# Optimization experiments

Measured on AMD Instinct MI355X. Metric: run time of the kernel, lower is better.

The kernel has to match this reference:

```python
import jax, jax.numpy as jnp
import numpy as np

EMBED_DIM = 1024
NUM_HEADS = 16
HEAD_DIM = EMBED_DIM // NUM_HEADS


def setup_inputs() -> dict:
    key = jax.random.key(0)
    ks = jax.random.split(key, 9)
    B, S, D = 4, 2048, EMBED_DIM
    scale = 1.0 / np.sqrt(D)
    x = jax.random.normal(ks[0], (B, S, D), dtype=jnp.float32)
    Wq = jax.random.normal(ks[1], (D, D), dtype=jnp.float32) * scale
    bq = jax.random.normal(ks[2], (D,), dtype=jnp.float32) * 0.01
    Wk = jax.random.normal(ks[3], (D, D), dtype=jnp.float32) * scale
    bk = jax.random.normal(ks[4], (D,), dtype=jnp.float32) * 0.01
    Wv = jax.random.normal(ks[5], (D, D), dtype=jnp.float32) * scale
    bv = jax.random.normal(ks[6], (D,), dtype=jnp.float32) * 0.01
    Wo = jax.random.normal(ks[7], (D, D), dtype=jnp.float32) * scale
    bo = jax.random.normal(ks[8], (D,), dtype=jnp.float32) * 0.01
    return {"x": x, "Wq": Wq, "bq": bq, "Wk": Wk, "bk": bk,
            "Wv": Wv, "bv": bv, "Wo": Wo, "bo": bo}


def reference(x, Wq, bq, Wk, bk, Wv, bv, Wo, bo):
    # Self-attention (kv = input). torch Linear: y = x @ W.T + b
    B, S, D = x.shape
    H, Dh = NUM_HEADS, HEAD_DIM
    q = (x @ Wq.T + bq).reshape(B, S, H, Dh).transpose(0, 2, 1, 3)  # [B,H,S,Dh]
    k = (x @ Wk.T + bk).reshape(B, S, H, Dh).transpose(0, 2, 1, 3)
    v = (x @ Wv.T + bv).reshape(B, S, H, Dh).transpose(0, 2, 1, 3)
    scale = 1.0 / jnp.sqrt(jnp.asarray(Dh, dtype=x.dtype))
    scores = jnp.einsum("bhsd,bhtd->bhst", q, k) * scale  # [B,H,S,S]
    causal = jnp.tril(jnp.ones((S, S), dtype=bool))        # True = keep
    scores = jnp.where(causal, scores, jnp.asarray(-jnp.inf, dtype=scores.dtype))
    attn = jax.nn.softmax(scores, axis=-1)
    out = jnp.einsum("bhst,bhtd->bhsd", attn, v)           # [B,H,S,Dh]
    out = out.transpose(0, 2, 1, 3).reshape(B, S, D)
    return out @ Wo.T + bo
```

## Files before the change

kernel.cpp:

```cpp
#include <hip/hip_runtime.h>

#define DMODEL 1024
#define NH     16
#define DH     64
#define BATCH  4
#define SEQ    2048
#define NROWS  (BATCH*SEQ)
#define QTILES (SEQ/256)

typedef short    s16x8  __attribute__((ext_vector_type(8)));
typedef float    f32x4  __attribute__((ext_vector_type(4)));
typedef float    f32x16 __attribute__((ext_vector_type(16)));
typedef unsigned u32x4  __attribute__((ext_vector_type(4)));

#define MFMA16 __builtin_amdgcn_mfma_f32_16x16x32_bf16
#define MFMA32 __builtin_amdgcn_mfma_f32_32x32x16_bf16

__device__ __forceinline__ unsigned short f2bf(float f) {
    unsigned u = __builtin_bit_cast(unsigned, f);
    return (unsigned short)((u + 0x7FFFu + ((u >> 16) & 1u)) >> 16);
}
__device__ __forceinline__ float bf2f(unsigned short s) {
    return __builtin_bit_cast(float, (unsigned)s << 16);
}
__device__ __forceinline__ unsigned pk2(unsigned short a, unsigned short b) {
    return (unsigned)a | ((unsigned)b << 16);
}
__device__ __forceinline__ void split4(float4 v, unsigned& h0, unsigned& h1,
                                       unsigned& l0, unsigned& l1) {
    unsigned short hx=f2bf(v.x), hy=f2bf(v.y), hz=f2bf(v.z), hw=f2bf(v.w);
    h0 = pk2(hx,hy); h1 = pk2(hz,hw);
    l0 = pk2(f2bf(v.x-bf2f(hx)), f2bf(v.y-bf2f(hy)));
    l1 = pk2(f2bf(v.z-bf2f(hz)), f2bf(v.w-bf2f(hw)));
}

#define LDK 40

__global__ __launch_bounds__(256, 2)
void qkv_kernel(const float* __restrict__ x,
                const float* __restrict__ Wq, const float* __restrict__ bq,
                const float* __restrict__ Wk, const float* __restrict__ bk,
                const float* __restrict__ Wv, const float* __restrict__ bv,
                float* __restrict__ qo, float* __restrict__ ko, float* __restrict__ vo)
{
    const int bmi = blockIdx.x;
    const int bn  = blockIdx.y;
    const int mat = bn >> 3;
    const float* __restrict__ W    = (mat == 0) ? Wq : (mat == 1) ? Wk : Wv;
    const float* __restrict__ bias = (mat == 0) ? bq : (mat == 1) ? bk : bv;
    float* __restrict__ out        = (mat == 0) ? qo : (mat == 1) ? ko : vo;
    const int m0 = bmi * 128;
    const int c0 = (bn & 7) * 128;

    __shared__ unsigned short Ah[128][LDK], Al[128][LDK];
    __shared__ unsigned short Bh[128][LDK], Bl[128][LDK];

    const int t    = threadIdx.x;
    const int srow = t >> 1;
    const int skc  = (t & 1) * 16;
    const int lane = t & 63;
    const int wid  = t >> 6;
    const int wm   = (wid >> 1) * 64;
    const int wn   = (wid & 1) * 64;
    const int fr   = lane & 15;
    const int fk   = (lane >> 4) * 8;

    const float* pa = &x[(size_t)(m0 + srow)*DMODEL + skc];
    const float* pb = &W[(size_t)(c0 + srow)*DMODEL + skc];

    f32x4 acc[4][4];
    #pragma unroll
    for (int i = 0; i < 4; ++i)
        #pragma unroll
        for (int j = 0; j < 4; ++j)
            #pragma unroll
            for (int e = 0; e < 4; ++e) acc[i][j][e] = 0.f;

    float4 av[4], bv4[4];
    #pragma unroll
    for (int i = 0; i < 4; ++i) { av[i] = *(const float4*)(pa + 4*i); bv4[i] = *(const float4*)(pb + 4*i); }

    for (int k0 = 0; k0 < DMODEL; k0 += 32) {
        __syncthreads();
        #pragma unroll
        for (int i = 0; i < 4; ++i) {
            unsigned h0,h1,l0,l1;
            split4(av[i], h0,h1,l0,l1);
            *(unsigned*)&Ah[srow][skc+4*i]   = h0;  *(unsigned*)&Ah[srow][skc+4*i+2] = h1;
            *(unsigned*)&Al[srow][skc+4*i]   = l0;  *(unsigned*)&Al[srow][skc+4*i+2] = l1;
            split4(bv4[i], h0,h1,l0,l1);
            *(unsigned*)&Bh[srow][skc+4*i]   = h0;  *(unsigned*)&Bh[srow][skc+4*i+2] = h1;
            *(unsigned*)&Bl[srow][skc+4*i]   = l0;  *(unsigned*)&Bl[srow][skc+4*i+2] = l1;
        }
        __syncthreads();

        const int kn = (k0 + 32 < DMODEL) ? k0 + 32 : 0;
        #pragma unroll
        for (int i = 0; i < 4; ++i) { av[i] = *(const float4*)(pa + kn + 4*i); bv4[i] = *(const float4*)(pb + kn + 4*i); }

        s16x8 a_hi[4], a_lo[4], b_hi[4], b_lo[4];
        #pragma unroll
        for (int i = 0; i < 4; ++i) {
            a_hi[i] = *(const s16x8*)&Ah[wm + i*16 + fr][fk];
            a_lo[i] = *(const s16x8*)&Al[wm + i*16 + fr][fk];
            b_hi[i] = *(const s16x8*)&Bh[wn + i*16 + fr][fk];
            b_lo[i] = *(const s16x8*)&Bl[wn + i*16 + fr][fk];
        }
        #pragma unroll
        for (int i = 0; i < 4; ++i)
            #pragma unroll
            for (int j = 0; j < 4; ++j) {
                acc[i][j] = MFMA16(a_hi[i], b_hi[j], acc[i][j], 0, 0, 0);
                acc[i][j] = MFMA16(a_hi[i], b_lo[j], acc[i][j], 0, 0, 0);
                acc[i][j] = MFMA16(a_lo[i], b_hi[j], acc[i][j], 0, 0, 0);
            }
    }

    const int rbase = m0 + wm + (lane >> 4) * 4;
    #pragma unroll
    for (int j = 0; j < 4; ++j) {
        const int cidx = c0 + wn + j*16 + fr;
        const float bb = bias[cidx];
        const int hd = cidx >> 6;
        const int dh = cidx & 63;
        #pragma unroll
        for (int i = 0; i < 4; ++i)
            #pragma unroll
            for (int r4 = 0; r4 < 4; ++r4) {
                const int r = rbase + i*16 + r4;
                const int b = r >> 11;
                const int s = r & (SEQ - 1);
                out[((size_t)(b*NH + hd)*SEQ + s)*DH + dh] = acc[i][j][r4] + bb;
            }
    }
}

#define LDKK 72
#define LDVT 74

__global__ __launch_bounds__(256, 2)
void attn_kernel(const float* __restrict__ qg, const float* __restrict__ kg,
                 const float* __restrict__ vg, float* __restrict__ out)
{
    const int bx = blockIdx.x, bh = blockIdx.y;
    const int qt = (bh & 32) ? bx : (QTILES - 1 - bx);
    const int t  = threadIdx.x;
    const int w  = t >> 6;
    const int lane = t & 63;
    const int h  = lane >> 5;
    const int c  = lane & 31;
    const int q0 = qt * 256;
    const int wq0 = q0 + w * 64;

    __shared__ unsigned short Kh[64][LDKK], Kl[64][LDKK];
    __shared__ unsigned short Vth[64][LDVT], Vtl[64][LDVT];
    __shared__ float l_lds[4][64];

    s16x8 qfh[2][4], qfl[2][4];
    #pragma unroll
    for (int qrt = 0; qrt < 2; ++qrt)
        #pragma unroll
        for (int s = 0; s < 4; ++s) {
            const float* qp = qg + ((size_t)bh*SEQ + (wq0 + qrt*32 + c))*DH + s*16 + h*8;
            u32x4 hw, lw;
            #pragma unroll
            for (int p2 = 0; p2 < 4; ++p2) {
                const float f0 = 0.125f * qp[2*p2];
                const float f1 = 0.125f * qp[2*p2+1];
                const unsigned short b0 = f2bf(f0), b1 = f2bf(f1);
                hw[p2] = pk2(b0, b1);
                lw[p2] = pk2(f2bf(f0 - bf2f(b0)), f2bf(f1 - bf2f(b1)));
            }
            qfh[qrt][s] = __builtin_bit_cast(s16x8, hw);
            qfl[qrt][s] = __builtin_bit_cast(s16x8, lw);
        }

    f32x16 oacc[2][2];
    #pragma unroll
    for (int i = 0; i < 2; ++i)
        #pragma unroll
        for (int j = 0; j < 2; ++j)
            #pragma unroll
            for (int e = 0; e < 16; ++e) oacc[i][j][e] = 0.f;
    float lsum0 = 0.f, lsum1 = 0.f;

    const float* kbase = kg + (size_t)bh*SEQ*DH;
    const float* vbase = vg + (size_t)bh*SEQ*DH;
    const int wlim = wq0 + 64;

    for (int kb = 0; kb < q0 + 256; kb += 64) {
        __syncthreads();
        const float4* kt4 = (const float4*)(kbase + (size_t)kb*DH);
        #pragma unroll
        for (int i = 0; i < 4; ++i) {
            const int f = t + i*256;
            const int key = f >> 4;
            const int d4  = (f & 15) * 4;
            unsigned h0,h1,l0,l1;
            split4(kt4[f], h0,h1,l0,l1);
            *(unsigned*)&Kh[key][d4]   = h0;  *(unsigned*)&Kh[key][d4+2] = h1;
            *(unsigned*)&Kl[key][d4]   = l0;  *(unsigned*)&Kl[key][d4+2] = l1;
        }
        const float* vt0 = vbase + (size_t)kb*DH;
        #pragma unroll
        for (int j = 0; j < 16; ++j) {
            const int key = w + 4*j;
            const float vv = vt0[(size_t)key*DH + lane];
            const unsigned short hb = f2bf(vv);
            Vth[lane][key] = hb;
            Vtl[lane][key] = f2bf(vv - bf2f(hb));
        }
        __syncthreads();

        if (kb < wlim) {
            f32x16 sac[2][2];
            #pragma unroll
            for (int i = 0; i < 2; ++i)
                #pragma unroll
                for (int j = 0; j < 2; ++j)
                    #pragma unroll
                    for (int e = 0; e < 16; ++e) sac[i][j][e] = 0.f;

            #pragma unroll
            for (int s = 0; s < 4; ++s) {
                s16x8 akh[2], akl[2];
                #pragma unroll
                for (int kt = 0; kt < 2; ++kt) {
                    akh[kt] = *(const s16x8*)&Kh[kt*32 + c][s*16 + h*8];
                    akl[kt] = *(const s16x8*)&Kl[kt*32 + c][s*16 + h*8];
                }
                #pragma unroll
                for (int kt = 0; kt < 2; ++kt)
                    #pragma unroll
                    for (int qrt = 0; qrt < 2; ++qrt) {
                        sac[kt][qrt] = MFMA32(akh[kt], qfh[qrt][s], sac[kt][qrt], 0,0,0);
                        sac[kt][qrt] = MFMA32(akh[kt], qfl[qrt][s], sac[kt][qrt], 0,0,0);
                        sac[kt][qrt] = MFMA32(akl[kt], qfh[qrt][s], sac[kt][qrt], 0,0,0);
                    }
            }

            const bool diag = (kb == wq0);
            float ps0 = 0.f, ps1 = 0.f;
            #pragma unroll
            for (int kt = 0; kt < 2; ++kt)
                #pragma unroll
                for (int qrt = 0; qrt < 2; ++qrt)
                    #pragma unroll
                    for (int r = 0; r < 16; ++r) {
                        float p = __expf(sac[kt][qrt][r] - 8.0f);
                        if (diag) {
                            const int key = kb + kt*32 + (r & 3) + ((r >> 2) << 3) + h*4;
                            const int qr  = wq0 + qrt*32 + c;
                            p = (key <= qr) ? p : 0.f;
                        }
                        sac[kt][qrt][r] = p;
                        if (qrt == 0) ps0 += p; else ps1 += p;
                    }
            lsum0 += ps0; lsum1 += ps1;

            #pragma unroll
            for (int s = 0; s < 4; ++s) {
                const int kt = s >> 1;
                const int rb = (s & 1) * 8;
                s16x8 pfh[2], pfl[2];
                #pragma unroll
                for (int qrt = 0; qrt < 2; ++qrt) {
                    unsigned short ph[8], pl[8];
                    #pragma unroll
                    for (int j = 0; j < 8; ++j) {
                        const float p = sac[kt][qrt][rb + j];
                        const unsigned short hb = f2bf(p);
                        ph[j] = hb;
                        pl[j] = f2bf(p - bf2f(hb));
                    }
                    const unsigned G0h0 = pk2(ph[0],ph[1]), G0h1 = pk2(ph[2],ph[3]);
                    const unsigned G1h0 = pk2(ph[4],ph[5]), G1h1 = pk2(ph[6],ph[7]);
                    const unsigned G0l0 = pk2(pl[0],pl[1]), G0l1 = pk2(pl[2],pl[3]);
                    const unsigned G1l0 = pk2(pl[4],pl[5]), G1l1 = pk2(pl[6],pl[7]);
                    const unsigned sG0h0 = __shfl_xor(G0h0, 32, 64), sG0h1 = __shfl_xor(G0h1, 32, 64);
                    const unsigned sG1h0 = __shfl_xor(G1h0, 32, 64), sG1h1 = __shfl_xor(G1h1, 32, 64);
                    const unsigned sG0l0 = __shfl_xor(G0l0, 32, 64), sG0l1 = __shfl_xor(G0l1, 32, 64);
                    const unsigned sG1l0 = __shfl_xor(G1l0, 32, 64), sG1l1 = __shfl_xor(G1l1, 32, 64);
                    u32x4 fh, fl;
                    if (h == 0) {
                        fh[0]=G0h0;  fh[1]=G0h1;  fh[2]=sG0h0; fh[3]=sG0h1;
                        fl[0]=G0l0;  fl[1]=G0l1;  fl[2]=sG0l0; fl[3]=sG0l1;
                    } else {
                        fh[0]=sG1h0; fh[1]=sG1h1; fh[2]=G1h0;  fh[3]=G1h1;
                        fl[0]=sG1l0; fl[1]=sG1l1; fl[2]=G1l0;  fl[3]=G1l1;
                    }
                    pfh[qrt] = __builtin_bit_cast(s16x8, fh);
                    pfl[qrt] = __builtin_bit_cast(s16x8, fl);
                }
                #pragma unroll
                for (int dt = 0; dt < 2; ++dt) {
                    const unsigned short* vhp = &Vth[dt*32 + c][s*16 + h*8];
                    const unsigned short* vlp = &Vtl[dt*32 + c][s*16 + h*8];
                    u32x4 wh, wl;
                    #pragma unroll
                    for (int u = 0; u < 4; ++u) {
                        wh[u] = *(const unsigned*)(vhp + 2*u);
                        wl[u] = *(const unsigned*)(vlp + 2*u);
                    }
                    const s16x8 vfh = __builtin_bit_cast(s16x8, wh);
                    const s16x8 vfl = __builtin_bit_cast(s16x8, wl);
                    #pragma unroll
                    for (int qrt = 0; qrt < 2; ++qrt) {
                        oacc[qrt][dt] = MFMA32(pfh[qrt], vfh, oacc[qrt][dt], 0,0,0);
                        oacc[qrt][dt] = MFMA32(pfh[qrt], vfl, oacc[qrt][dt], 0,0,0);
                        oacc[qrt][dt] = MFMA32(pfl[qrt], vfh, oacc[qrt][dt], 0,0,0);
                    }
                }
            }
        }
    }

    lsum0 += __shfl_xor(lsum0, 32, 64);
    lsum1 += __shfl_xor(lsum1, 32, 64);
    l_lds[w][c]      = lsum0;
    l_lds[w][32 + c] = lsum1;
    __syncthreads();

    const int b = bh >> 4, hd = bh & 15;
    #pragma unroll
    for (int qrt = 0; qrt < 2; ++qrt)
        #pragma unroll
        for (int r = 0; r < 16; ++r) {
            const int qloc = qrt*32 + (r & 3) + ((r >> 2) << 3) + h*4;
            const float linv = 1.f / l_lds[w][qloc];
            float* op = out + ((size_t)(b*SEQ + wq0 + qloc))*DMODEL + hd*DH;
            op[c]      = oacc[qrt][0][r] * linv;
            op[32 + c] = oacc[qrt][1][r] * linv;
        }
}

__global__ __launch_bounds__(256, 2)
void proj_kernel(const float* __restrict__ A, const float* __restrict__ W,
                 const float* __restrict__ bias, float* __restrict__ out)
{
    const int m0 = blockIdx.x * 128;
    const int c0 = blockIdx.y * 128;

    __shared__ unsigned short Ah[128][LDK], Al[128][LDK];
    __shared__ unsigned short Bh[128][LDK], Bl[128][LDK];

    const int t    = threadIdx.x;
    const int srow = t >> 1;
    const int skc  = (t & 1) * 16;
    const int lane = t & 63;
    const int wid  = t >> 6;
    const int wm   = (wid >> 1) * 64;
    const int wn   = (wid & 1) * 64;
    const int fr   = lane & 15;
    const int fk   = (lane >> 4) * 8;

    const float* pa = &A[(size_t)(m0 + srow)*DMODEL + skc];
    const float* pb = &W[(size_t)(c0 + srow)*DMODEL + skc];

    f32x4 acc[4][4];
    #pragma unroll
    for (int i = 0; i < 4; ++i)
        #pragma unroll
        for (int j = 0; j < 4; ++j)
            #pragma unroll
            for (int e = 0; e < 4; ++e) acc[i][j][e] = 0.f;

    float4 av[4], bv4[4];
    #pragma unroll
    for (int i = 0; i < 4; ++i) { av[i] = *(const float4*)(pa + 4*i); bv4[i] = *(const float4*)(pb + 4*i); }

    for (int k0 = 0; k0 < DMODEL; k0 += 32) {
        __syncthreads();
        #pragma unroll
        for (int i = 0; i < 4; ++i) {
            unsigned h0,h1,l0,l1;
            split4(av[i], h0,h1,l0,l1);
            *(unsigned*)&Ah[srow][skc+4*i]   = h0;  *(unsigned*)&Ah[srow][skc+4*i+2] = h1;
            *(unsigned*)&Al[srow][skc+4*i]   = l0;  *(unsigned*)&Al[srow][skc+4*i+2] = l1;
            split4(bv4[i], h0,h1,l0,l1);
            *(unsigned*)&Bh[srow][skc+4*i]   = h0;  *(unsigned*)&Bh[srow][skc+4*i+2] = h1;
            *(unsigned*)&Bl[srow][skc+4*i]   = l0;  *(unsigned*)&Bl[srow][skc+4*i+2] = l1;
        }
        __syncthreads();

        const int kn = (k0 + 32 < DMODEL) ? k0 + 32 : 0;
        #pragma unroll
        for (int i = 0; i < 4; ++i) { av[i] = *(const float4*)(pa + kn + 4*i); bv4[i] = *(const float4*)(pb + kn + 4*i); }

        s16x8 a_hi[4], a_lo[4], b_hi[4], b_lo[4];
        #pragma unroll
        for (int i = 0; i < 4; ++i) {
            a_hi[i] = *(const s16x8*)&Ah[wm + i*16 + fr][fk];
            a_lo[i] = *(const s16x8*)&Al[wm + i*16 + fr][fk];
            b_hi[i] = *(const s16x8*)&Bh[wn + i*16 + fr][fk];
            b_lo[i] = *(const s16x8*)&Bl[wn + i*16 + fr][fk];
        }
        #pragma unroll
        for (int i = 0; i < 4; ++i)
            #pragma unroll
            for (int j = 0; j < 4; ++j) {
                acc[i][j] = MFMA16(a_hi[i], b_hi[j], acc[i][j], 0, 0, 0);
                acc[i][j] = MFMA16(a_hi[i], b_lo[j], acc[i][j], 0, 0, 0);
                acc[i][j] = MFMA16(a_lo[i], b_hi[j], acc[i][j], 0, 0, 0);
            }
    }

    const int rbase = m0 + wm + (lane >> 4) * 4;
    #pragma unroll
    for (int j = 0; j < 4; ++j) {
        const int cidx = c0 + wn + j*16 + fr;
        const float bb = bias[cidx];
        #pragma unroll
        for (int i = 0; i < 4; ++i)
            #pragma unroll
            for (int r4 = 0; r4 < 4; ++r4) {
                const int r = rbase + i*16 + r4;
                out[(size_t)r*DMODEL + cidx] = acc[i][j][r4] + bb;
            }
    }
}

extern "C" void kernel_launch(void* const* d_in, const int* in_sizes, int n_in,
                              void* d_out, int out_size, void* d_ws, size_t ws_size,
                              hipStream_t stream)
{
    const float* x  = (const float*)d_in[0];
    const float* Wq = (const float*)d_in[1];
    const float* bq = (const float*)d_in[2];
    const float* Wk = (const float*)d_in[3];
    const float* bk = (const float*)d_in[4];
    const float* Wv = (const float*)d_in[5];
    const float* bv = (const float*)d_in[6];
    const float* Wo = (const float*)d_in[7];
    const float* bo = (const float*)d_in[8];
    float* out = (float*)d_out;

    float* ws = (float*)d_ws;
    const size_t SZ = (size_t)NROWS * DMODEL;
    float* q  = ws;
    float* k  = ws + SZ;
    float* v  = ws + 2*SZ;
    float* ao = ws + 3*SZ;

    dim3 g1(NROWS/128, 24);
    qkv_kernel<<<g1, 256, 0, stream>>>(x, Wq, bq, Wk, bk, Wv, bv, q, k, v);

    dim3 g2(QTILES, BATCH*NH);
    attn_kernel<<<g2, 256, 0, stream>>>(q, k, v, ao);

    dim3 g3(NROWS/128, DMODEL/128);
    proj_kernel<<<g3, 256, 0, stream>>>(ao, Wo, bo, out);
}
```

Baseline: 553.0 us.

## Store intermediates as pre-split bf16 hi/lo pairs and double-buffer attention K/V tiles

Adds a pre-pass that splits x into bf16 hi/lo halves. The QKV projection now emits Q, K and a transposed V directly as bf16 hi/lo pairs, and attention writes its output the same way. This removes the repeated fp32-to-bf16 split work inside the GEMM and attention inner loops and lets those loops copy tiles with vector loads. Attention also double-buffers its K/V shared-memory tiles with register prefetch, so it syncs once per iteration, and the 1/8 Q scale moves into the exp argument. The cost is an extra kernel launch, a pass over x, and scattered 2-byte stores for the transposed V.

```diff
diff --git a/kernel.cpp b/kernel.cpp
--- a/kernel.cpp
+++ b/kernel.cpp
@@ -8,65 +8,99 @@
 #define NROWS  (BATCH*SEQ)
 #define QTILES (SEQ/256)
 
+typedef unsigned short u16;
+typedef unsigned int   u32;
 typedef short    s16x8  __attribute__((ext_vector_type(8)));
 typedef float    f32x4  __attribute__((ext_vector_type(4)));
 typedef float    f32x16 __attribute__((ext_vector_type(16)));
 typedef unsigned u32x4  __attribute__((ext_vector_type(4)));
+typedef unsigned u32x2  __attribute__((ext_vector_type(2)));
 
 #define MFMA16 __builtin_amdgcn_mfma_f32_16x16x32_bf16
 #define MFMA32 __builtin_amdgcn_mfma_f32_32x32x16_bf16
 
-__device__ __forceinline__ unsigned short f2bf(float f) {
-    unsigned u = __builtin_bit_cast(unsigned, f);
-    return (unsigned short)((u + 0x7FFFu + ((u >> 16) & 1u)) >> 16);
-}
-__device__ __forceinline__ float bf2f(unsigned short s) {
-    return __builtin_bit_cast(float, (unsigned)s << 16);
-}
-__device__ __forceinline__ unsigned pk2(unsigned short a, unsigned short b) {
-    return (unsigned)a | ((unsigned)b << 16);
-}
-__device__ __forceinline__ void split4(float4 v, unsigned& h0, unsigned& h1,
-                                       unsigned& l0, unsigned& l1) {
-    unsigned short hx=f2bf(v.x), hy=f2bf(v.y), hz=f2bf(v.z), hw=f2bf(v.w);
-    h0 = pk2(hx,hy); h1 = pk2(hz,hw);
-    l0 = pk2(f2bf(v.x-bf2f(hx)), f2bf(v.y-bf2f(hy)));
-    l1 = pk2(f2bf(v.z-bf2f(hz)), f2bf(v.w-bf2f(hw)));
+__device__ __forceinline__ u16 f2bf(float f) {
+    u32 u = __builtin_bit_cast(u32, f);
+    return (u16)((u + 0x7FFFu + ((u >> 16) & 1u)) >> 16);
+}
+__device__ __forceinline__ float bf2f(u16 s) {
+    return __builtin_bit_cast(float, (u32)s << 16);
+}
+__device__ __forceinline__ u32 pk2(u16 a, u16 b) {
+    return (u32)a | ((u32)b << 16);
+}
+__device__ __forceinline__ void split16(const float4* f4, u32x4& h0, u32x4& h1,
+                                        u32x4& l0, u32x4& l1) {
+    float f[16];
+    #pragma unroll
+    for (int i = 0; i < 4; ++i) { f[4*i]=f4[i].x; f[4*i+1]=f4[i].y; f[4*i+2]=f4[i].z; f[4*i+3]=f4[i].w; }
+    u32 hw[8], lw[8];
+    #pragma unroll
+    for (int u = 0; u < 8; ++u) {
+        const u16 a = f2bf(f[2*u]), b = f2bf(f[2*u+1]);
+        hw[u] = pk2(a, b);
+        lw[u] = pk2(f2bf(f[2*u] - bf2f(a)), f2bf(f[2*u+1] - bf2f(b)));
+    }
+    h0 = (u32x4){hw[0],hw[1],hw[2],hw[3]}; h1 = (u32x4){hw[4],hw[5],hw[6],hw[7]};
+    l0 = (u32x4){lw[0],lw[1],lw[2],lw[3]}; l1 = (u32x4){lw[4],lw[5],lw[6],lw[7]};
+}
+
+__global__ __launch_bounds__(256)
+void split_x_kernel(const float* __restrict__ x, u16* __restrict__ xh, u16* __restrict__ xl)
+{
+    const int n4 = NROWS*DMODEL/4;
+    for (int i = blockIdx.x*256 + threadIdx.x; i < n4; i += gridDim.x*256) {
+        const float4 v = ((const float4*)x)[i];
+        float f[4] = {v.x, v.y, v.z, v.w};
+        u32 h[2], l[2];
+        #pragma unroll
+        for (int u = 0; u < 2; ++u) {
+            const u16 a = f2bf(f[2*u]), b = f2bf(f[2*u+1]);
+            h[u] = pk2(a, b);
+            l[u] = pk2(f2bf(f[2*u] - bf2f(a)), f2bf(f[2*u+1] - bf2f(b)));
+        }
+        *(u32x2*)&xh[4*i] = (u32x2){h[0], h[1]};
+        *(u32x2*)&xl[4*i] = (u32x2){l[0], l[1]};
+    }
 }
 
 #define LDK 40
 
 __global__ __launch_bounds__(256, 2)
-void qkv_kernel(const float* __restrict__ x,
+void qkv_kernel(const u16* __restrict__ xh, const u16* __restrict__ xl,
                 const float* __restrict__ Wq, const float* __restrict__ bq,
                 const float* __restrict__ Wk, const float* __restrict__ bk,
                 const float* __restrict__ Wv, const float* __restrict__ bv,
-                float* __restrict__ qo, float* __restrict__ ko, float* __restrict__ vo)
+                u16* __restrict__ qh, u16* __restrict__ ql,
+                u16* __restrict__ kh, u16* __restrict__ kl,
+                u16* __restrict__ vth, u16* __restrict__ vtl)
 {
     const int bmi = blockIdx.x;
     const int bn  = blockIdx.y;
     const int mat = bn >> 3;
     const float* __restrict__ W    = (mat == 0) ? Wq : (mat == 1) ? Wk : Wv;
     const float* __restrict__ bias = (mat == 0) ? bq : (mat == 1) ? bk : bv;
-    float* __restrict__ out        = (mat == 0) ? qo : (mat == 1) ? ko : vo;
     const int m0 = bmi * 128;
     const int c0 = (bn & 7) * 128;
 
-    __shared__ unsigned short Ah[128][LDK], Al[128][LDK];
-    __shared__ unsigned short Bh[128][LDK], Bl[128][LDK];
+    __shared__ u16 Ah[128][LDK], Al[128][LDK];
+    __shared__ u16 Bh[128][LDK], Bl[128][LDK];
 
     const int t    = threadIdx.x;
-    const int srow = t >> 1;
-    const int skc  = (t & 1) * 16;
     const int lane = t & 63;
     const int wid  = t >> 6;
     const int wm   = (wid >> 1) * 64;
     const int wn   = (wid & 1) * 64;
     const int fr   = lane & 15;
     const int fk   = (lane >> 4) * 8;
-
-    const float* pa = &x[(size_t)(m0 + srow)*DMODEL + skc];
-    const float* pb = &W[(size_t)(c0 + srow)*DMODEL + skc];
+    const int ar  = t >> 2;
+    const int ac  = (t & 3) * 8;
+    const int srow = t >> 1;
+    const int skc  = (t & 1) * 16;
+
+    const u16*   pah = &xh[(size_t)(m0 + ar)*DMODEL + ac];
+    const u16*   pal = &xl[(size_t)(m0 + ar)*DMODEL + ac];
+    const float* pb  = &W[(size_t)(c0 + srow)*DMODEL + skc];
 
     f32x4 acc[4][4];
     #pragma unroll
@@ -76,27 +110,36 @@
             #pragma unroll
             for (int e = 0; e < 4; ++e) acc[i][j][e] = 0.f;
 
-    float4 av[4], bv4[4];
-    #pragma unroll
-    for (int i = 0; i < 4; ++i) { av[i] = *(const float4*)(pa + 4*i); bv4[i] = *(const float4*)(pb + 4*i); }
+    u32x4 ra0, ra1, ra2, ra3;
+    float4 rb[4];
+    ra0 = *(const u32x4*)(pah);
+    ra1 = *(const u32x4*)(pah + (size_t)64*DMODEL);
+    ra2 = *(const u32x4*)(pal);
+    ra3 = *(const u32x4*)(pal + (size_t)64*DMODEL);
+    #pragma unroll
+    for (int i = 0; i < 4; ++i) rb[i] = *(const float4*)(pb + 4*i);
 
     for (int k0 = 0; k0 < DMODEL; k0 += 32) {
         __syncthreads();
-        #pragma unroll
-        for (int i = 0; i < 4; ++i) {
-            unsigned h0,h1,l0,l1;
-            split4(av[i], h0,h1,l0,l1);
-            *(unsigned*)&Ah[srow][skc+4*i]   = h0;  *(unsigned*)&Ah[srow][skc+4*i+2] = h1;
-            *(unsigned*)&Al[srow][skc+4*i]   = l0;  *(unsigned*)&Al[srow][skc+4*i+2] = l1;
-            split4(bv4[i], h0,h1,l0,l1);
-            *(unsigned*)&Bh[srow][skc+4*i]   = h0;  *(unsigned*)&Bh[srow][skc+4*i+2] = h1;
-            *(unsigned*)&Bl[srow][skc+4*i]   = l0;  *(unsigned*)&Bl[srow][skc+4*i+2] = l1;
-        }
+        *(u32x4*)&Ah[ar][ac]      = ra0;
+        *(u32x4*)&Ah[ar + 64][ac] = ra1;
+        *(u32x4*)&Al[ar][ac]      = ra2;
+        *(u32x4*)&Al[ar + 64][ac] = ra3;
+        u32x4 h0, h1, l0, l1;
+        split16(rb, h0, h1, l0, l1);
+        *(u32x4*)&Bh[srow][skc]     = h0;
+        *(u32x4*)&Bh[srow][skc + 8] = h1;
+        *(u32x4*)&Bl[srow][skc]     = l0;
+        *(u32x4*)&Bl[srow][skc + 8] = l1;
         __syncthreads();
 
         const int kn = (k0 + 32 < DMODEL) ? k0 + 32 : 0;
-        #pragma unroll
-        for (int i = 0; i < 4; ++i) { av[i] = *(const float4*)(pa + kn + 4*i); bv4[i] = *(const float4*)(pb + kn + 4*i); }
+        ra0 = *(const u32x4*)(pah + kn);
+        ra1 = *(const u32x4*)(pah + kn + (size_t)64*DMODEL);
+        ra2 = *(const u32x4*)(pal + kn);
+        ra3 = *(const u32x4*)(pal + kn + (size_t)64*DMODEL);
+        #pragma unroll
+        for (int i = 0; i < 4; ++i) rb[i] = *(const float4*)(pb + kn + 4*i);
 
         s16x8 a_hi[4], a_lo[4], b_hi[4], b_lo[4];
         #pragma unroll
@@ -130,17 +173,30 @@
                 const int r = rbase + i*16 + r4;
                 const int b = r >> 11;
                 const int s = r & (SEQ - 1);
-                out[((size_t)(b*NH + hd)*SEQ + s)*DH + dh] = acc[i][j][r4] + bb;
-            }
-    }
-}
-
-#define LDKK 72
-#define LDVT 74
+                const float v = acc[i][j][r4] + bb;
+                const u16 hb = f2bf(v);
+                const u16 lb = f2bf(v - bf2f(hb));
+                if (mat == 2) {
+                    const size_t idx = ((size_t)(b*NH + hd)*DH + dh)*SEQ + s;
+                    vth[idx] = hb; vtl[idx] = lb;
+                } else if (mat == 1) {
+                    const size_t idx = ((size_t)(b*NH + hd)*SEQ + s)*DH + dh;
+                    kh[idx] = hb; kl[idx] = lb;
+                } else {
+                    const size_t idx = ((size_t)(b*NH + hd)*SEQ + s)*DH + dh;
+                    qh[idx] = hb; ql[idx] = lb;
+                }
+            }
+    }
+}
+
+#define LDA 72
 
 __global__ __launch_bounds__(256, 2)
-void attn_kernel(const float* __restrict__ qg, const float* __restrict__ kg,
-                 const float* __restrict__ vg, float* __restrict__ out)
+void attn_kernel(const u16* __restrict__ qh, const u16* __restrict__ ql,
+                 const u16* __restrict__ kh, const u16* __restrict__ kl,
+                 const u16* __restrict__ vth, const u16* __restrict__ vtl,
+                 u16* __restrict__ aoh, u16* __restrict__ aol)
 {
     const int bx = blockIdx.x, bh = blockIdx.y;
     const int qt = (bh & 32) ? bx : (QTILES - 1 - bx);
@@ -151,28 +207,25 @@
     const int c  = lane & 31;
     const int q0 = qt * 256;
     const int wq0 = q0 + w * 64;
-
-    __shared__ unsigned short Kh[64][LDKK], Kl[64][LDKK];
-    __shared__ unsigned short Vth[64][LDVT], Vtl[64][LDVT];
+    const int wlim = wq0 + 64;
+
+    __shared__ u16 Kh[2][64][LDA], Kl[2][64][LDA];
+    __shared__ u16 Vh[2][64][LDA], Vl[2][64][LDA];
     __shared__ float l_lds[4][64];
 
+    const int sr = t >> 3;
+    const int sc = (t & 7) * 8;
+    const size_t krow = (size_t)bh * SEQ;
+    const size_t vrow = (size_t)bh * DH;
+
     s16x8 qfh[2][4], qfl[2][4];
     #pragma unroll
     for (int qrt = 0; qrt < 2; ++qrt)
         #pragma unroll
         for (int s = 0; s < 4; ++s) {
-            const float* qp = qg + ((size_t)bh*SEQ + (wq0 + qrt*32 + c))*DH + s*16 + h*8;
-            u32x4 hw, lw;
-            #pragma unroll
-            for (int p2 = 0; p2 < 4; ++p2) {
-                const float f0 = 0.125f * qp[2*p2];
-                const float f1 = 0.125f * qp[2*p2+1];
-                const unsigned short b0 = f2bf(f0), b1 = f2bf(f1);
-                hw[p2] = pk2(b0, b1);
-                lw[p2] = pk2(f2bf(f0 - bf2f(b0)), f2bf(f1 - bf2f(b1)));
-            }
-            qfh[qrt][s] = __builtin_bit_cast(s16x8, hw);
-            qfl[qrt][s] = __builtin_bit_cast(s16x8, lw);
+            const size_t qi = (krow + (wq0 + qrt*32 + c))*DH + s*16 + h*8;
+            qfh[qrt][s] = *(const s16x8*)&qh[qi];
+            qfl[qrt][s] = *(const s16x8*)&ql[qi];
         }
 
     f32x16 oacc[2][2];
@@ -184,33 +237,36 @@
             for (int e = 0; e < 16; ++e) oacc[i][j][e] = 0.f;
     float lsum0 = 0.f, lsum1 = 0.f;
 
-    const float* kbase = kg + (size_t)bh*SEQ*DH;
-    const float* vbase = vg + (size_t)bh*SEQ*DH;
-    const int wlim = wq0 + 64;
+    u32x4 pk[8];
+#define LOADT(KB) do { \
+    pk[0] = *(const u32x4*)&kh[(krow + (KB) + sr)*DH + sc];        \
+    pk[1] = *(const u32x4*)&kh[(krow + (KB) + sr + 32)*DH + sc];   \
+    pk[2] = *(const u32x4*)&kl[(krow + (KB) + sr)*DH + sc];        \
+    pk[3] = *(const u32x4*)&kl[(krow + (KB) + sr + 32)*DH + sc];   \
+    pk[4] = *(const u32x4*)&vth[(vrow + sr)*SEQ + (KB) + sc];      \
+    pk[5] = *(const u32x4*)&vth[(vrow + sr + 32)*SEQ + (KB) + sc]; \
+    pk[6] = *(const u32x4*)&vtl[(vrow + sr)*SEQ + (KB) + sc];      \
+    pk[7] = *(const u32x4*)&vtl[(vrow + sr + 32)*SEQ + (KB) + sc]; \
+} while (0)
+#define STORET(B) do { \
+    *(u32x4*)&Kh[B][sr][sc]      = pk[0]; \
+    *(u32x4*)&Kh[B][sr + 32][sc] = pk[1]; \
+    *(u32x4*)&Kl[B][sr][sc]      = pk[2]; \
+    *(u32x4*)&Kl[B][sr + 32][sc] = pk[3]; \
+    *(u32x4*)&Vh[B][sr][sc]      = pk[4]; \
+    *(u32x4*)&Vh[B][sr + 32][sc] = pk[5]; \
+    *(u32x4*)&Vl[B][sr][sc]      = pk[6]; \
+    *(u32x4*)&Vl[B][sr + 32][sc] = pk[7]; \
+} while (0)
+
+    LOADT(0);
+    STORET(0);
+    __syncthreads();
+    int cur = 0;
 
     for (int kb = 0; kb < q0 + 256; kb += 64) {
-        __syncthreads();
-        const float4* kt4 = (const float4*)(kbase + (size_t)kb*DH);
-        #pragma unroll
-        for (int i = 0; i < 4; ++i) {
-            const int f = t + i*256;
-            const int key = f >> 4;
-            const int d4  = (f & 15) * 4;
-            unsigned h0,h1,l0,l1;
-            split4(kt4[f], h0,h1,l0,l1);
-            *(unsigned*)&Kh[key][d4]   = h0;  *(unsigned*)&Kh[key][d4+2] = h1;
-            *(unsigned*)&Kl[key][d4]   = l0;  *(unsigned*)&Kl[key][d4+2] = l1;
-        }
-        const float* vt0 = vbase + (size_t)kb*DH;
-        #pragma unroll
-        for (int j = 0; j < 16; ++j) {
-            const int key = w + 4*j;
-            const float vv = vt0[(size_t)key*DH + lane];
-            const unsigned short hb = f2bf(vv);
-            Vth[lane][key] = hb;
-            Vtl[lane][key] = f2bf(vv - bf2f(hb));
-        }
-        __syncthreads();
+        const bool hasnext = (kb + 64 < q0 + 256);
+        if (hasnext) LOADT(kb + 64);
 
         if (kb < wlim) {
             f32x16 sac[2][2];
@@ -226,8 +282,8 @@
                 s16x8 akh[2], akl[2];
                 #pragma unroll
                 for (int kt = 0; kt < 2; ++kt) {
-                    akh[kt] = *(const s16x8*)&Kh[kt*32 + c][s*16 + h*8];
-                    akl[kt] = *(const s16x8*)&Kl[kt*32 + c][s*16 + h*8];
+                    akh[kt] = *(const s16x8*)&Kh[cur][kt*32 + c][s*16 + h*8];
+                    akl[kt] = *(const s16x8*)&Kl[cur][kt*32 + c][s*16 + h*8];
                 }
                 #pragma unroll
                 for (int kt = 0; kt < 2; ++kt)
@@ -247,7 +303,7 @@
                 for (int qrt = 0; qrt < 2; ++qrt)
                     #pragma unroll
                     for (int r = 0; r < 16; ++r) {
-                        float p = __expf(sac[kt][qrt][r] - 8.0f);
+                        float p = __expf(fmaf(sac[kt][qrt][r], 0.125f, -8.0f));
                         if (diag) {
                             const int key = kb + kt*32 + (r & 3) + ((r >> 2) << 3) + h*4;
                             const int qr  = wq0 + qrt*32 + c;
@@ -265,22 +321,22 @@
                 s16x8 pfh[2], pfl[2];
                 #pragma unroll
                 for (int qrt = 0; qrt < 2; ++qrt) {
-                    unsigned short ph[8], pl[8];
+                    u16 ph[8], pl[8];
                     #pragma unroll
                     for (int j = 0; j < 8; ++j) {
                         const float p = sac[kt][qrt][rb + j];
-                        const unsigned short hb = f2bf(p);
+                        const u16 hb = f2bf(p);
                         ph[j] = hb;
                         pl[j] = f2bf(p - bf2f(hb));
                     }
-                    const unsigned G0h0 = pk2(ph[0],ph[1]), G0h1 = pk2(ph[2],ph[3]);
-                    const unsigned G1h0 = pk2(ph[4],ph[5]), G1h1 = pk2(ph[6],ph[7]);
-                    const unsigned G0l0 = pk2(pl[0],pl[1]), G0l1 = pk2(pl[2],pl[3]);
-                    const unsigned G1l0 = pk2(pl[4],pl[5]), G1l1 = pk2(pl[6],pl[7]);
-                    const unsigned sG0h0 = __shfl_xor(G0h0, 32, 64), sG0h1 = __shfl_xor(G0h1, 32, 64);
-                    const unsigned sG1h0 = __shfl_xor(G1h0, 32, 64), sG1h1 = __shfl_xor(G1h1, 32, 64);
-                    const unsigned sG0l0 = __shfl_xor(G0l0, 32, 64), sG0l1 = __shfl_xor(G0l1, 32, 64);
-                    const unsigned sG1l0 = __shfl_xor(G1l0, 32, 64), sG1l1 = __shfl_xor(G1l1, 32, 64);
+                    const u32 G0h0 = pk2(ph[0],ph[1]), G0h1 = pk2(ph[2],ph[3]);
+                    const u32 G1h0 = pk2(ph[4],ph[5]), G1h1 = pk2(ph[6],ph[7]);
+                    const u32 G0l0 = pk2(pl[0],pl[1]), G0l1 = pk2(pl[2],pl[3]);
+                    const u32 G1l0 = pk2(pl[4],pl[5]), G1l1 = pk2(pl[6],pl[7]);
+                    const u32 sG0h0 = __shfl_xor(G0h0, 32, 64), sG0h1 = __shfl_xor(G0h1, 32, 64);
+                    const u32 sG1h0 = __shfl_xor(G1h0, 32, 64), sG1h1 = __shfl_xor(G1h1, 32, 64);
+                    const u32 sG0l0 = __shfl_xor(G0l0, 32, 64), sG0l1 = __shfl_xor(G0l1, 32, 64);
+                    const u32 sG1l0 = __shfl_xor(G1l0, 32, 64), sG1l1 = __shfl_xor(G1l1, 32, 64);
                     u32x4 fh, fl;
                     if (h == 0) {
                         fh[0]=G0h0;  fh[1]=G0h1;  fh[2]=sG0h0; fh[3]=sG0h1;
@@ -294,16 +350,8 @@
                 }
                 #pragma unroll
                 for (int dt = 0; dt < 2; ++dt) {
-                    const unsigned short* vhp = &Vth[dt*32 + c][s*16 + h*8];
-                    const unsigned short* vlp = &Vtl[dt*32 + c][s*16 + h*8];
-                    u32x4 wh, wl;
-                    #pragma unroll
-                    for (int u = 0; u < 4; ++u) {
-                        wh[u] = *(const unsigned*)(vhp + 2*u);
-                        wl[u] = *(const unsigned*)(vlp + 2*u);
-                    }
-                    const s16x8 vfh = __builtin_bit_cast(s16x8, wh);
-                    const s16x8 vfl = __builtin_bit_cast(s16x8, wl);
+                    const s16x8 vfh = *(const s16x8*)&Vh[cur][dt*32 + c][s*16 + h*8];
+                    const s16x8 vfl = *(const s16x8*)&Vl[cur][dt*32 + c][s*16 + h*8];
                     #pragma unroll
                     for (int qrt = 0; qrt < 2; ++qrt) {
                         oacc[qrt][dt] = MFMA32(pfh[qrt], vfh, oacc[qrt][dt], 0,0,0);
@@ -313,6 +361,10 @@
                 }
             }
         }
+
+        if (hasnext) STORET(cur ^ 1);
+        __syncthreads();
+        cur ^= 1;
     }
 
     lsum0 += __shfl_xor(lsum0, 32, 64);
@@ -328,34 +380,43 @@
         for (int r = 0; r < 16; ++r) {
             const int qloc = qrt*32 + (r & 3) + ((r >> 2) << 3) + h*4;
             const float linv = 1.f / l_lds[w][qloc];
-            float* op = out + ((size_t)(b*SEQ + wq0 + qloc))*DMODEL + hd*DH;
-            op[c]      = oacc[qrt][0][r] * linv;
-            op[32 + c] = oacc[qrt][1][r] * linv;
+            const size_t rowi = ((size_t)(b*SEQ + wq0 + qloc))*DMODEL + hd*DH;
+            #pragma unroll
+            for (int dt = 0; dt < 2; ++dt) {
+                const float ov = oacc[qrt][dt][r] * linv;
+                const u16 hb = f2bf(ov);
+                aoh[rowi + dt*32 + c] = hb;
+                aol[rowi + dt*32 + c] = f2bf(ov - bf2f(hb));
+            }
         }
 }
 
 __global__ __launch_bounds__(256, 2)
-void proj_kernel(const float* __restrict__ A, const float* __restrict__ W,
-                 const float* __restrict__ bias, float* __restrict__ out)
+void proj_kernel(const u16* __restrict__ aoh, const u16* __restrict__ aol,
+                 const float* __restrict__ W, const float* __restrict__ bias,
+                 float* __restrict__ out)
 {
     const int m0 = blockIdx.x * 128;
     const int c0 = blockIdx.y * 128;
 
-    __shared__ unsigned short Ah[128][LDK], Al[128][LDK];
-    __shared__ unsigned short Bh[128][LDK], Bl[128][LDK];
+    __shared__ u16 Ah[128][LDK], Al[128][LDK];
+    __shared__ u16 Bh[128][LDK], Bl[128][LDK];
 
     const int t    = threadIdx.x;
-    const int srow = t >> 1;
-    const int skc  = (t & 1) * 16;
     const int lane = t & 63;
     const int wid  = t >> 6;
     const int wm   = (wid >> 1) * 64;
     const int wn   = (wid & 1) * 64;
     const int fr   = lane & 15;
     const int fk   = (lane >> 4) * 8;
-
-    const float* pa = &A[(size_t)(m0 + srow)*DMODEL + skc];
-    const float* pb = &W[(size_t)(c0 + srow)*DMODEL + skc];
+    const int ar   = t >> 2;
+    const int ac   = (t & 3) * 8;
+    const int srow = t >> 1;
+    const int skc  = (t & 1) * 16;
+
+    const u16*   pah = &aoh[(size_t)(m0 + ar)*DMODEL + ac];
+    const u16*   pal = &aol[(size_t)(m0 + ar)*DMODEL + ac];
+    const float* pb  = &W[(size_t)(c0 + srow)*DMODEL + skc];
 
     f32x4 acc[4][4];
     #pragma unroll
@@ -365,27 +426,35 @@
             #pragma unroll
             for (int e = 0; e < 4; ++e) acc[i][j][e] = 0.f;
 
-    float4 av[4], bv4[4];
-    #pragma unroll
-    for (int i = 0; i < 4; ++i) { av[i] = *(const float4*)(pa + 4*i); bv4[i] = *(const float4*)(pb + 4*i); }
+    u32x4 ra0 = *(const u32x4*)(pah);
+    u32x4 ra1 = *(const u32x4*)(pah + (size_t)64*DMODEL);
+    u32x4 ra2 = *(const u32x4*)(pal);
+    u32x4 ra3 = *(const u32x4*)(pal + (size_t)64*DMODEL);
+    float4 rb[4];
+    #pragma unroll
+    for (int i = 0; i < 4; ++i) rb[i] = *(const float4*)(pb + 4*i);
 
     for (int k0 = 0; k0 < DMODEL; k0 += 32) {
         __syncthreads();
-        #pragma unroll
-        for (int i = 0; i < 4; ++i) {
-            unsigned h0,h1,l0,l1;
-            split4(av[i], h0,h1,l0,l1);
-            *(unsigned*)&Ah[srow][skc+4*i]   = h0;  *(unsigned*)&Ah[srow][skc+4*i+2] = h1;
-            *(unsigned*)&Al[srow][skc+4*i]   = l0;  *(unsigned*)&Al[srow][skc+4*i+2] = l1;
-            split4(bv4[i], h0,h1,l0,l1);
-            *(unsigned*)&Bh[srow][skc+4*i]   = h0;  *(unsigned*)&Bh[srow][skc+4*i+2] = h1;
-            *(unsigned*)&Bl[srow][skc+4*i]   = l0;  *(unsigned*)&Bl[srow][skc+4*i+2] = l1;
-        }
+        *(u32x4*)&Ah[ar][ac]      = ra0;
+        *(u32x4*)&Ah[ar + 64][ac] = ra1;
+        *(u32x4*)&Al[ar][ac]      = ra2;
+        *(u32x4*)&Al[ar + 64][ac] = ra3;
+        u32x4 h0, h1, l0, l1;
+        split16(rb, h0, h1, l0, l1);
+        *(u32x4*)&Bh[srow][skc]     = h0;
+        *(u32x4*)&Bh[srow][skc + 8] = h1;
+        *(u32x4*)&Bl[srow][skc]     = l0;
+        *(u32x4*)&Bl[srow][skc + 8] = l1;
         __syncthreads();
 
         const int kn = (k0 + 32 < DMODEL) ? k0 + 32 : 0;
-        #pragma unroll
-        for (int i = 0; i < 4; ++i) { av[i] = *(const float4*)(pa + kn + 4*i); bv4[i] = *(const float4*)(pb + kn + 4*i); }
+        ra0 = *(const u32x4*)(pah + kn);
+        ra1 = *(const u32x4*)(pah + kn + (size_t)64*DMODEL);
+        ra2 = *(const u32x4*)(pal + kn);
+        ra3 = *(const u32x4*)(pal + kn + (size_t)64*DMODEL);
+        #pragma unroll
+        for (int i = 0; i < 4; ++i) rb[i] = *(const float4*)(pb + kn + 4*i);
 
         s16x8 a_hi[4], a_lo[4], b_hi[4], b_lo[4];
         #pragma unroll
@@ -435,19 +504,23 @@
     const float* bo = (const float*)d_in[8];
     float* out = (float*)d_out;
 
-    float* ws = (float*)d_ws;
-    const size_t SZ = (size_t)NROWS * DMODEL;
-    float* q  = ws;
-    float* k  = ws + SZ;
-    float* v  = ws + 2*SZ;
-    float* ao = ws + 3*SZ;
+    u16* wsp = (u16*)d_ws;
+    const size_t NE = (size_t)NROWS * DMODEL;
+    u16* xh  = wsp;           u16* xl  = wsp + NE;
+    u16* aoh = wsp;           u16* aol = wsp + NE;
+    u16* qh  = wsp + 2*NE;    u16* ql  = wsp + 3*NE;
+    u16* kh  = wsp + 4*NE;    u16* kl  = wsp + 5*NE;
+    u16* vth = wsp + 6*NE;    u16* vtl = wsp + 7*NE;
+
+    split_x_kernel<<<2048, 256, 0, stream>>>(x, xh, xl);
 
     dim3 g1(NROWS/128, 24);
-    qkv_kernel<<<g1, 256, 0, stream>>>(x, Wq, bq, Wk, bk, Wv, bv, q, k, v);
+    qkv_kernel<<<g1, 256, 0, stream>>>(xh, xl, Wq, bq, Wk, bk, Wv, bv,
+                                       qh, ql, kh, kl, vth, vtl);
 
     dim3 g2(QTILES, BATCH*NH);
-    attn_kernel<<<g2, 256, 0, stream>>>(q, k, v, ao);
+    attn_kernel<<<g2, 256, 0, stream>>>(qh, ql, kh, kl, vth, vtl, aoh, aol);
 
     dim3 g3(NROWS/128, DMODEL/128);
-    proj_kernel<<<g3, 256, 0, stream>>>(ao, Wo, bo, out);
-}
+    proj_kernel<<<g3, 256, 0, stream>>>(aoh, aol, Wo, bo, out);
+}
```

After: 547.5 us. Within noise of the previous version (-1.0%).
